# Optimization experiments

Hardware: AMD Instinct MI355X
Metric: run time of the kernel (lower is better)

## Reference

```python
import jax, jax.numpy as jnp
import numpy as np

N_HEADS = 12
MAX_POS = 2048
SEQ = MAX_POS - 2  # seq_len_without_special = 2046
HEAD_DIM = 64
BATCH = 8


def setup_inputs() -> dict:
    key = jax.random.key(0)
    k1, k2, k3 = jax.random.split(key, 3)
    v = jax.random.normal(k1, (BATCH, MAX_POS, N_HEADS, HEAD_DIM), jnp.float32)
    offset = jax.random.normal(k2, (1, N_HEADS), jnp.float32)
    # learned bias base, torch init: uniform(-0.1, 0.1), shape [1, H, SEQ] (symmetric)
    w = jax.random.uniform(k3, (1, N_HEADS, SEQ), jnp.float32, -0.1, 0.1)
    return {"v": v, "offset": offset, "w": w}


def _fft_bias(v, offset, w):
    # strip special tokens ([CLS]/[SEP])
    v_ = v[:, 1:-1, :, :]                      # [B, S, H, D]
    B, S, H, D = v_.shape
    # --- symmetric circulant base z of length 2S-1 ---
    w_ = w[..., :S]                            # [1, H, S]
    z = jnp.concatenate(
        [w_[..., -1:], jnp.flip(w_[..., 1:], axis=-1), w_[..., :-1]], axis=-1
    )                                          # [1, H, 2S-1]
    z = z - offset[..., None]                  # broadcast offset per head
    z = jnp.exp(z)                             # feature_map == 'exp'
    z_fft = jnp.fft.rfft(z)                    # [1, H, S] complex (len 2S-1 odd -> m=S)

    pad = S - 1                                # symmetric: pad_size = seq_len - 1
    v_p = jnp.transpose(v_, (0, 3, 2, 1))      # [B, D, H, S]
    v_p = jnp.pad(v_p, ((0, 0), (0, 0), (0, 0), (pad, 0)))  # left-pad to 2S-1
    v_fft = jnp.fft.rfft(v_p)                  # [B, D, H, S]
    # torch.irfft(x, 1) with default signal_sizes infers even length 2*(m-1)=2S-2
    pbv = jnp.fft.irfft(v_fft * z_fft)[..., :S]  # [B, D, H, S]
    pbv = jnp.pad(pbv, ((0, 0), (0, 0), (0, 0), (1, 1)))     # restore special slots
    pbv = jnp.transpose(pbv, (0, 3, 2, 1))     # [B, S+2, H, D]

    o = jnp.pad(jnp.ones((S,), v.dtype), (pad, 0))           # [2S-1]
    o_fft = jnp.fft.rfft(o)                    # [S]
    z_pb = jnp.fft.irfft(z_fft * o_fft)[..., :S]             # [1, H, S]
    z_pb = jnp.pad(z_pb, ((0, 0), (0, 0), (1, 1)))           # [1, H, S+2]
    z_pb = jnp.swapaxes(z_pb, -2, -1)          # [1, S+2, H]
    return pbv, z_pb


def reference(v, offset, w):
    return _fft_bias(v, offset, w)
```

## Files before the change

### kernel.cpp

```cpp
#include <hip/hip_runtime.h>
#include <hip/hip_bf16.h>

#define BATCH 8
#define MAXPOS 2048
#define SEQ 2046
#define NH 12
#define HD 64
#define NCSLOT 254
#define TSTEPS 64
#define PLANE (NH * HD)

typedef __attribute__((ext_vector_type(4))) float floatx4;
typedef __attribute__((ext_vector_type(8))) short shortx8;

#define ATILE_BYTES (NH * NCSLOT * 512 * 2)

#define GLOAD_LDS16(src, dst)                                                  \
    __builtin_amdgcn_global_load_lds(                                          \
        (const __attribute__((address_space(1))) void*)(src),                  \
        (__attribute__((address_space(3))) void*)(dst), 16, 0, 0)

#define NB_V   (TSTEPS * NH * BATCH)
#define NB_ZPB NH
#define NB_A   (NCSLOT * NH)

__global__ __launch_bounds__(256)
void prep_all(const float* __restrict__ v, const float* __restrict__ w,
              const float* __restrict__ off, ushort* __restrict__ atile,
              ushort* __restrict__ vbf, float* __restrict__ out) {
    const int bi  = blockIdx.x;
    const int tid = threadIdx.x;

    if (bi < NB_V) {
        __shared__ float Ls[32][64];
        const int tc = bi & 63;
        int rem = bi >> 6;
        const int h = rem % NH;
        const int b = rem / NH;
#pragma unroll
        for (int i = 0; i < 2; ++i) {
            int idx = tid + 256 * i;
            int row = idx >> 4;
            int c4  = (idx & 15) * 4;
            int key = (row >> 3) * 16;
            int t   = tc * 32 + row;
            float4 val = make_float4(0.f, 0.f, 0.f, 0.f);
            if (t < SEQ) val = *(const float4*)(v + ((size_t)(b * MAXPOS + 1 + t) * NH + h) * HD + c4);
            *(float4*)&Ls[row][c4 ^ key] = val;
        }
        __syncthreads();
        const int wv   = tid >> 6;
        const int lane = tid & 63;
        const int q    = lane >> 4;
        const int dcol = lane & 15;
        ushort pk[8];
#pragma unroll
        for (int j = 0; j < 8; ++j) {
            __hip_bfloat16 bv = __float2bfloat16(Ls[q * 8 + j][(wv * 16 + dcol) ^ (q * 16)]);
            pk[j] = *(ushort*)&bv;
        }
        *(uint4*)(vbf + ((size_t)((b * NH + h) * TSTEPS + tc) * 4 + wv) * 512 + lane * 8) = *(uint4*)pk;
    } else if (bi < NB_V + NB_ZPB) {
        __shared__ float Es[SEQ];
        __shared__ float Ss[SEQ];
        __shared__ float wsum[4];
        const int h    = bi - NB_V;
        const int wid  = tid >> 6;
        const int lane = tid & 63;
        const float offh = off[h];
        const float* wh  = w + h * SEQ;
        for (int i = tid; i < SEQ; i += 256) Es[i] = __expf(wh[i] - offh);
        __syncthreads();
        const int base = tid * 8;
        float loc[8];
        float s = 0.f;
#pragma unroll
        for (int j = 0; j < 8; ++j) {
            float e = (base + j < SEQ) ? Es[base + j] : 0.f;
            s += e; loc[j] = s;
        }
        float sc = s;
#pragma unroll
        for (int d = 1; d < 64; d <<= 1) {
            float t = __shfl_up(sc, d);
            if (lane >= d) sc += t;
        }
        if (lane == 63) wsum[wid] = sc;
        __syncthreads();
        float woff = 0.f;
        for (int k = 0; k < wid; ++k) woff += wsum[k];
        float prefix = woff + sc - s;
#pragma unroll
        for (int j = 0; j < 8; ++j)
            if (base + j < SEQ) Ss[base + j] = prefix + loc[j];
        __syncthreads();
        const float E0 = Es[0];
        const size_t zb = (size_t)BATCH * MAXPOS * PLANE;
        for (int i = tid; i < SEQ; i += 256)
            out[zb + (size_t)(i + 1) * NH + h] = Ss[i] + Ss[SEQ - 1 - i] - E0;
    } else if (bi < NB_V + NB_ZPB + NB_A) {
        const int idx   = bi - NB_V - NB_ZPB;
        const int cslot = idx % NCSLOT;
        const int h     = idx / NCSLOT;
        const float offh = off[h];
        const float* wh  = w + h * SEQ;
        const int ci   = cslot - 127;
        const int lane = tid >> 2;
        const int jp   = (tid & 3) * 2;
        const int q    = lane >> 4;
        const int m    = lane & 15;
        const int d0   = 16 * ci + q * 8 - m + jp;
        ushort pk[2];
#pragma unroll
        for (int e = 0; e < 2; ++e) {
            int k = d0 + e; k = (k < 0) ? -k : k;
            float val = (k < SEQ) ? __expf(wh[k] - offh) : 0.f;
            __hip_bfloat16 bv = __float2bfloat16(val);
            pk[e] = *(ushort*)&bv;
        }
        *(ushort2*)(atile + ((size_t)(h * NCSLOT + cslot) * 512 + lane * 8 + jp)) = *(ushort2*)pk;
    } else {
        const int i = (bi - NB_V - NB_ZPB - NB_A) * 256 + tid;
        if (i < 2 * BATCH * PLANE) {
            int side = i / (BATCH * PLANE);
            int r    = i % (BATCH * PLANE);
            int b    = r / PLANE;
            int j    = r % PLANE;
            int p    = side ? (MAXPOS - 1) : 0;
            out[((size_t)b * MAXPOS + p) * PLANE + j] = 0.f;
        }
        if (i < 2 * NH) {
            size_t zb = (size_t)BATCH * MAXPOS * PLANE;
            int p = (i < NH) ? 0 : (MAXPOS - 1);
            out[zb + (size_t)p * NH + (i % NH)] = 0.f;
        }
    }
}

__global__ __launch_bounds__(256, 3)
void gemm_pbv(const ushort* __restrict__ atile, const ushort* __restrict__ vbf,
              float* __restrict__ out) {
    __shared__ short As[2][8 * 512];

    const int bid  = blockIdx.x;
    const int slot = bid >> 3;
    const int g    = (bid & 7) * 6 + (slot % 6);
    const int nt   = slot / 6;
    const int h    = g >> 2;
    const int bq   = g & 3;
    const int tid  = threadIdx.x;
    const int wv   = tid >> 6;
    const int lane = tid & 63;
    const int sh   = wv >> 1;
    const int bw   = wv & 1;
    const int bb   = bq * 2 + bw;

    floatx4 acc[4][4];
#pragma unroll
    for (int s = 0; s < 4; ++s)
#pragma unroll
        for (int dt = 0; dt < 4; ++dt) acc[s][dt] = (floatx4){0.f, 0.f, 0.f, 0.f};

    const ushort* aS = atile + ((size_t)h * NCSLOT + (127 - nt * 8 - 2 * wv)) * 512 + lane * 8;
    const ushort* bP = vbf + (size_t)(bb * NH + h) * (TSTEPS * 4 * 512) + lane * 8;
    short* aW0 = &As[0][2 * wv * 512];
    short* aW1 = &As[1][2 * wv * 512];
    const short* aR0 = &As[0][sh * 4 * 512] + lane * 8;
    const short* aR1 = &As[1][sh * 4 * 512] + lane * 8;

    shortx8 a[4], b0[4], b1[4];

    GLOAD_LDS16(aS, aW0);
    GLOAD_LDS16(aS - 512, aW0 + 512);
#pragma unroll
    for (int dt = 0; dt < 4; ++dt) b0[dt] = *(const shortx8*)(bP + dt * 512);
    __syncthreads();

    for (int tc = 0; tc < TSTEPS; tc += 2) {
        GLOAD_LDS16(aS + (tc + 1) * 1024, aW1);
        GLOAD_LDS16(aS + (tc + 1) * 1024 - 512, aW1 + 512);
#pragma unroll
        for (int dt = 0; dt < 4; ++dt)
            b1[dt] = *(const shortx8*)(bP + (tc + 1) * 2048 + dt * 512);
#pragma unroll
        for (int s = 0; s < 4; ++s) a[s] = *(const shortx8*)(aR0 + s * 512);
#pragma unroll
        for (int s = 0; s < 4; ++s)
#pragma unroll
            for (int dt = 0; dt < 4; ++dt)
                acc[s][dt] = __builtin_amdgcn_mfma_f32_16x16x32_bf16(a[s], b0[dt], acc[s][dt], 0, 0, 0);
        __syncthreads();

        if (tc + 2 < TSTEPS) {
            GLOAD_LDS16(aS + (tc + 2) * 1024, aW0);
            GLOAD_LDS16(aS + (tc + 2) * 1024 - 512, aW0 + 512);
#pragma unroll
            for (int dt = 0; dt < 4; ++dt)
                b0[dt] = *(const shortx8*)(bP + (tc + 2) * 2048 + dt * 512);
        }
#pragma unroll
        for (int s = 0; s < 4; ++s) a[s] = *(const shortx8*)(aR1 + s * 512);
#pragma unroll
        for (int s = 0; s < 4; ++s)
#pragma unroll
            for (int dt = 0; dt < 4; ++dt)
                acc[s][dt] = __builtin_amdgcn_mfma_f32_16x16x32_bf16(a[s], b1[dt], acc[s][dt], 0, 0, 0);
        __syncthreads();
    }

    const int q    = lane >> 4;
    const int dcol = lane & 15;
    const int nB   = nt * 128 + sh * 64;
#pragma unroll
    for (int s = 0; s < 4; ++s) {
        int nsb = nB + s * 16 + q * 4;
#pragma unroll
        for (int r = 0; r < 4; ++r) {
            int n = nsb + r;
            if (n < SEQ) {
                float* ob = out + ((size_t)(bb * MAXPOS + 1 + n) * NH + h) * HD + dcol;
#pragma unroll
                for (int dt = 0; dt < 4; ++dt) ob[dt * 16] = acc[s][dt][r];
            }
        }
    }
}

extern "C" void kernel_launch(void* const* d_in, const int* in_sizes, int n_in,
                              void* d_out, int out_size, void* d_ws, size_t ws_size,
                              hipStream_t stream) {
    const float* v   = (const float*)d_in[0];
    const float* off = (const float*)d_in[1];
    const float* w   = (const float*)d_in[2];
    float* out = (float*)d_out;

    ushort* atile = (ushort*)d_ws;
    ushort* vbf   = (ushort*)((char*)d_ws + ATILE_BYTES);

    prep_all<<<NB_V + NB_ZPB + NB_A + 48, 256, 0, stream>>>(v, w, off, atile, vbf, out);
    gemm_pbv<<<768, 256, 0, stream>>>(atile, vbf, out);
}
```

Before: 146.7 us.

## Deepen GEMM pipeline to four LDS stages with partial vmcnt waits

Replaces the two-stage LDS double buffer in the bf16 MFMA GEMM with a four-slot ring that runs two steps ahead. The full __syncthreads is replaced by inline s_waitcnt vmcnt(6) plus s_barrier, so loads still in flight need not drain at each step. The loop is unrolled by four, and s_setprio is raised around the MFMA block. This aims to hide global-to-LDS latency, at the cost of doubled LDS use, which could reduce occupancy, and hand-tuned wait counts that must match the exact number of outstanding loads.

```diff
diff --git a/kernel.cpp b/kernel.cpp
--- a/kernel.cpp
+++ b/kernel.cpp
@@ -137,10 +137,40 @@
     }
 }
 
+
+#define FENCE    asm volatile("" ::: "memory")
+#define WAITBAR6 asm volatile("s_waitcnt vmcnt(6)\n\ts_barrier" ::: "memory")
+#define WAITBAR0 asm volatile("s_waitcnt vmcnt(0)\n\ts_barrier" ::: "memory")
+
+#define GEMM_STEP(CK, NXT, BS, STG)                                            \
+  do {                                                                         \
+    shortx8 aa[4];                                                             \
+    _Pragma("unroll")                                                          \
+    for (int s = 0; s < 4; ++s)                                                \
+        aa[s] = *(const shortx8*)(aRb + (CK) * 4096 + s * 512);                \
+    if (STG) {                                                                 \
+        GLOAD_LDS16(aQ + (CK) * 1024,       aWb + (NXT) * 4096);               \
+        GLOAD_LDS16(aQ + (CK) * 1024 - 512, aWb + (NXT) * 4096 + 512);         \
+    }                                                                          \
+    __builtin_amdgcn_s_setprio(1);                                             \
+    _Pragma("unroll")                                                          \
+    for (int s = 0; s < 4; ++s)                                                \
+        _Pragma("unroll")                                                      \
+        for (int dt = 0; dt < 4; ++dt)                                         \
+            acc[s][dt] = __builtin_amdgcn_mfma_f32_16x16x32_bf16(              \
+                aa[s], b[BS][dt], acc[s][dt], 0, 0, 0);                        \
+    __builtin_amdgcn_s_setprio(0);                                             \
+    if (STG) {                                                                 \
+        _Pragma("unroll")                                                      \
+        for (int dt = 0; dt < 4; ++dt)                                         \
+            b[BS][dt] = *(const shortx8*)(bQ + (CK) * 2048 + dt * 512);        \
+    }                                                                          \
+  } while (0)
+
 __global__ __launch_bounds__(256, 3)
 void gemm_pbv(const ushort* __restrict__ atile, const ushort* __restrict__ vbf,
               float* __restrict__ out) {
-    __shared__ short As[2][8 * 512];
+    __shared__ short As[4][8 * 512];
 
     const int bid  = blockIdx.x;
     const int slot = bid >> 3;
@@ -163,50 +193,37 @@
 
     const ushort* aS = atile + ((size_t)h * NCSLOT + (127 - nt * 8 - 2 * wv)) * 512 + lane * 8;
     const ushort* bP = vbf + (size_t)(bb * NH + h) * (TSTEPS * 4 * 512) + lane * 8;
-    short* aW0 = &As[0][2 * wv * 512];
-    short* aW1 = &As[1][2 * wv * 512];
-    const short* aR0 = &As[0][sh * 4 * 512] + lane * 8;
-    const short* aR1 = &As[1][sh * 4 * 512] + lane * 8;
-
-    shortx8 a[4], b0[4], b1[4];
-
-    GLOAD_LDS16(aS, aW0);
-    GLOAD_LDS16(aS - 512, aW0 + 512);
-#pragma unroll
-    for (int dt = 0; dt < 4; ++dt) b0[dt] = *(const shortx8*)(bP + dt * 512);
-    __syncthreads();
-
-    for (int tc = 0; tc < TSTEPS; tc += 2) {
-        GLOAD_LDS16(aS + (tc + 1) * 1024, aW1);
-        GLOAD_LDS16(aS + (tc + 1) * 1024 - 512, aW1 + 512);
-#pragma unroll
-        for (int dt = 0; dt < 4; ++dt)
-            b1[dt] = *(const shortx8*)(bP + (tc + 1) * 2048 + dt * 512);
-#pragma unroll
-        for (int s = 0; s < 4; ++s) a[s] = *(const shortx8*)(aR0 + s * 512);
-#pragma unroll
-        for (int s = 0; s < 4; ++s)
-#pragma unroll
-            for (int dt = 0; dt < 4; ++dt)
-                acc[s][dt] = __builtin_amdgcn_mfma_f32_16x16x32_bf16(a[s], b0[dt], acc[s][dt], 0, 0, 0);
-        __syncthreads();
-
-        if (tc + 2 < TSTEPS) {
-            GLOAD_LDS16(aS + (tc + 2) * 1024, aW0);
-            GLOAD_LDS16(aS + (tc + 2) * 1024 - 512, aW0 + 512);
-#pragma unroll
-            for (int dt = 0; dt < 4; ++dt)
-                b0[dt] = *(const shortx8*)(bP + (tc + 2) * 2048 + dt * 512);
-        }
-#pragma unroll
-        for (int s = 0; s < 4; ++s) a[s] = *(const shortx8*)(aR1 + s * 512);
-#pragma unroll
-        for (int s = 0; s < 4; ++s)
-#pragma unroll
-            for (int dt = 0; dt < 4; ++dt)
-                acc[s][dt] = __builtin_amdgcn_mfma_f32_16x16x32_bf16(a[s], b1[dt], acc[s][dt], 0, 0, 0);
-        __syncthreads();
+    short* aWb = &As[0][2 * wv * 512];
+    const short* aRb = &As[0][sh * 4 * 512] + lane * 8;
+
+    shortx8 b[2][4];
+
+    GLOAD_LDS16(aS,       aWb);
+    GLOAD_LDS16(aS - 512, aWb + 512);
+#pragma unroll
+    for (int dt = 0; dt < 4; ++dt) b[0][dt] = *(const shortx8*)(bP + dt * 512);
+    FENCE;
+    GLOAD_LDS16(aS + 1024, aWb + 4096);
+    GLOAD_LDS16(aS + 512,  aWb + 4096 + 512);
+#pragma unroll
+    for (int dt = 0; dt < 4; ++dt) b[1][dt] = *(const shortx8*)(bP + 2048 + dt * 512);
+    WAITBAR6;
+
+    const ushort* aQ = aS + 2 * 1024;
+    const ushort* bQ = bP + 2 * 2048;
+
+    for (int u = 0; u < 15; ++u) {
+        GEMM_STEP(0, 2, 0, 1); WAITBAR6;
+        GEMM_STEP(1, 3, 1, 1); WAITBAR6;
+        GEMM_STEP(2, 0, 0, 1); WAITBAR6;
+        GEMM_STEP(3, 1, 1, 1); WAITBAR6;
+        aQ += 4 * 1024;
+        bQ += 4 * 2048;
     }
+    GEMM_STEP(0, 2, 0, 1); WAITBAR6;
+    GEMM_STEP(1, 3, 1, 1); WAITBAR6;
+    GEMM_STEP(2, 0, 0, 0); WAITBAR0;
+    GEMM_STEP(3, 1, 1, 0);
 
     const int q    = lane >> 4;
     const int dcol = lane & 15;
```

After: 144.3 us. Within noise of the previous version (-1.6%).
